# Optimization experiments

Hardware: AMD Instinct MI355X
Metric: run time of the kernel (lower is better)

## Reference

```python
import jax, jax.numpy as jnp
import numpy as np

N_NODES = 100000
N_EDGES = 1600000
IN_FEATS = 128
N_HIDDEN = 32
N_CLASSES = 47
HEADS = (4, 4)
NEG_SLOPE = 0.2


def setup_inputs() -> dict:
    key = jax.random.key(0)
    ks = jax.random.split(key, 12)
    x = jax.random.normal(ks[0], (N_NODES, IN_FEATS), dtype=jnp.float32)
    src = jax.random.randint(ks[1], (N_EDGES,), 0, N_NODES)
    dst = jax.random.randint(ks[2], (N_EDGES,), 0, N_NODES)
    inverse_idx = jax.random.randint(ks[3], (N_NODES,), 0, N_NODES)
    h1 = HEADS[0] * N_HIDDEN
    s1 = 1.0 / np.sqrt(IN_FEATS)
    W1 = jax.random.normal(ks[4], (IN_FEATS, h1), dtype=jnp.float32) * s1
    al1 = jax.random.normal(ks[5], (HEADS[0], N_HIDDEN), dtype=jnp.float32) * 0.1
    ar1 = jax.random.normal(ks[6], (HEADS[0], N_HIDDEN), dtype=jnp.float32) * 0.1
    b1 = jnp.zeros((h1,), dtype=jnp.float32)
    h2 = HEADS[1] * N_CLASSES
    s2 = 1.0 / np.sqrt(h1)
    W2 = jax.random.normal(ks[7], (h1, h2), dtype=jnp.float32) * s2
    al2 = jax.random.normal(ks[8], (HEADS[1], N_CLASSES), dtype=jnp.float32) * 0.1
    ar2 = jax.random.normal(ks[9], (HEADS[1], N_CLASSES), dtype=jnp.float32) * 0.1
    b2 = jnp.zeros((h2,), dtype=jnp.float32)
    return {"x": x, "src": src, "dst": dst, "inverse_idx": inverse_idx,
            "W1": W1, "al1": al1, "ar1": ar1, "b1": b1,
            "W2": W2, "al2": al2, "ar2": ar2, "b2": b2}


def gat_conv(h, src, dst, W, al, ar, b, heads, out_dim, apply_elu):
    # DGL GATConv (feat_drop=attn_drop=0, eval mode):
    # projected per-head features, edge attention, per-dst softmax, aggregate.
    feat = (h @ W).reshape(-1, heads, out_dim)               # (N, H, D)
    el = jnp.einsum('nhd,hd->nh', feat, al)                  # (N, H)
    er = jnp.einsum('nhd,hd->nh', feat, ar)                  # (N, H)
    e = el[src] + er[dst]                                    # (E, H)
    e = jnp.where(e > 0, e, NEG_SLOPE * e)                   # LeakyReLU
    m = jax.ops.segment_max(e, dst, num_segments=N_NODES)    # (N, H)
    m = jnp.where(jnp.isfinite(m), m, 0.0)
    ex = jnp.exp(e - m[dst])
    s = jax.ops.segment_sum(ex, dst, num_segments=N_NODES)   # (N, H)
    alpha = ex / jnp.maximum(s[dst], 1e-9)                   # (E, H)
    msg = feat[src] * alpha[:, :, None]                      # (E, H, D)
    out = jax.ops.segment_sum(msg, dst, num_segments=N_NODES)  # (N, H, D)
    out = out + b.reshape(1, heads, out_dim)
    if apply_elu:
        out = jax.nn.elu(out)
    return out


def reference(x, src, dst, inverse_idx, W1, al1, ar1, b1, W2, al2, ar2, b2):
    # Layer 0: GATConv + ELU, flatten heads, then NPFeatureShuffle reindex.
    h = gat_conv(x, src, dst, W1, al1, ar1, b1, HEADS[0], N_HIDDEN, True)
    h = h.reshape(N_NODES, HEADS[0] * N_HIDDEN)
    h = h[inverse_idx]  # cross-partition shuffle reindex
    # Layer 1: GATConv, no activation, mean over heads.
    h = gat_conv(h, src, dst, W2, al2, ar2, b2, HEADS[1], N_CLASSES, False)
    return h.mean(axis=1)  # (N, n_classes)
```

## Files before the change

kernel.cpp:

```cpp
#include <hip/hip_runtime.h>
#include <hip/hip_bf16.h>
#include <hip/hip_fp16.h>
#include <type_traits>

#define N_NODES 100000
#define N_EDGES 1600000

typedef _Float16 half8_t __attribute__((ext_vector_type(8)));
typedef _Float16 half4_t __attribute__((ext_vector_type(4)));
typedef float floatx4 __attribute__((ext_vector_type(4)));

__global__ void csr_prep(const int* __restrict__ dst, int* __restrict__ deg, int E,
                         const float* __restrict__ W1, const float* __restrict__ W2,
                         const float* __restrict__ al1, const float* __restrict__ ar1,
                         const float* __restrict__ al2, const float* __restrict__ ar2,
                         __half* __restrict__ Wt1, __half* __restrict__ Wt2) {
    const int b = blockIdx.x;
    if (b < 6250) {
        int i = b * 256 + threadIdx.x;
        if (i < E) atomicAdd(&deg[dst[i]], 1);
        return;
    }
    const int c = b - 6250;
    const int k = threadIdx.x;
    if (k >= 128) return;
    if (c < 128) {
        Wt1[c * 128 + k] = __float2half(W1[k * 128 + c]);
    } else if (c < 144) {
        int j = c - 128;
        float v = 0.f;
        if (j < 8) {
            int h = j & 3;
            const float* a = (j < 4) ? al1 : ar1;
            for (int d = 0; d < 32; ++d)
                v = fmaf(W1[k * 128 + h * 32 + d], a[h * 32 + d], v);
        }
        Wt1[c * 128 + k] = __float2half(v);
    } else if (c < 336) {
        int c2 = c - 144;
        float v = (c2 < 188) ? W2[k * 188 + c2] : 0.f;
        Wt2[c2 * 128 + k] = __float2half(v);
    } else {
        int j = c - 336;
        float v = 0.f;
        if (j < 8) {
            int h = j & 3;
            const float* a = (j < 4) ? al2 : ar2;
            for (int d = 0; d < 47; ++d)
                v = fmaf(W2[k * 188 + h * 47 + d], a[h * 47 + d], v);
        }
        Wt2[(192 + j) * 128 + k] = __float2half(v);
    }
}

__global__ void block_sums(const int* __restrict__ deg, int* __restrict__ bsum, int N) {
    __shared__ int ws[4];
    const int t = threadIdx.x;
    int i = blockIdx.x * 256 + t;
    int v = (i < N) ? deg[i] : 0;
    #pragma unroll
    for (int o = 32; o; o >>= 1) v += __shfl_down(v, o, 64);
    if ((t & 63) == 0) ws[t >> 6] = v;
    __syncthreads();
    if (t == 0) bsum[blockIdx.x] = ws[0] + ws[1] + ws[2] + ws[3];
}

__global__ void scan_bsum(int* __restrict__ bsum, int nb) {
    __shared__ int sh[512];
    const int t = threadIdx.x;
    sh[t] = (t < nb) ? bsum[t] : 0;
    __syncthreads();
    for (int o = 1; o < 512; o <<= 1) {
        int v = (t >= o) ? sh[t - o] : 0;
        __syncthreads();
        sh[t] += v;
        __syncthreads();
    }
    if (t < nb) bsum[t] = sh[t];
}

__global__ void scan_final(const int* __restrict__ deg, const int* __restrict__ bsum,
                           int* __restrict__ row_ptr, int* __restrict__ cursor, int N) {
    __shared__ int ws[4];
    const int t = threadIdx.x;
    const int b = blockIdx.x;
    const int i = b * 256 + t;
    const int lane = t & 63;
    const int wid = t >> 6;
    int v = (i < N) ? deg[i] : 0;
    int x = v;
    #pragma unroll
    for (int o = 1; o < 64; o <<= 1) {
        int y = __shfl_up(x, o, 64);
        if (lane >= o) x += y;
    }
    if (lane == 63) ws[wid] = x;
    __syncthreads();
    int prefix = (b > 0) ? bsum[b - 1] : 0;
    for (int k = 0; k < wid; ++k) prefix += ws[k];
    if (i < N) {
        row_ptr[i + 1] = prefix + x;
        cursor[i] = prefix + x - v;
    }
    if (i == 0) row_ptr[0] = 0;
}

__global__ void scatter_edges_part(const int* __restrict__ src, const int* __restrict__ dst,
                                   int* __restrict__ cursor, int* __restrict__ e_src, int E) {
    const int part = blockIdx.x & 7;
    const int sb = blockIdx.x >> 3;
    const int nslices = gridDim.x >> 3;
    const int psz = N_NODES / 8;
    const int lo = part * psz;
    const int hi = (part == 7) ? N_NODES : lo + psz;
    const int begin = (int)((long long)E * sb / nslices);
    const int end = (int)((long long)E * (sb + 1) / nslices);
    for (int i = begin + threadIdx.x; i < end; i += blockDim.x) {
        int d = dst[i];
        if (d >= lo && d < hi) {
            int p = atomicAdd(&cursor[d], 1);
            e_src[p] = src[i];
        }
    }
}

template <int TT, int NLOG, int OSTRIDE, bool EMBED, bool GATHER, typename AT>
__global__ __launch_bounds__(256) void gemm_mfma(
    const AT* __restrict__ A, const __half* __restrict__ Wt,
    __half* __restrict__ C, __half* __restrict__ elh, float* __restrict__ er,
    const int* __restrict__ gather, int N) {
    constexpr int LDA = 136;
    __shared__ _Float16 As[64 * LDA];
    __shared__ int ridx[64];
    const int tid = threadIdx.x;
    const int r0 = blockIdx.x * 64;

    if (tid < 64) {
        int row = r0 + tid;
        int pr = 0;
        if (row < N) pr = GATHER ? gather[row] : row;
        ridx[tid] = pr;
    }
    __syncthreads();

    {
        const int r = tid >> 2, q = tid & 3;
        const int src = ridx[r];
        if constexpr (std::is_same<AT, float>::value) {
            const float4* A4 = (const float4*)A;
            #pragma unroll
            for (int i = 0; i < 8; ++i) {
                float4 v = A4[(size_t)src * 32 + q * 8 + i];
                half4_t hv = {(_Float16)v.x, (_Float16)v.y, (_Float16)v.z, (_Float16)v.w};
                *(half4_t*)&As[r * LDA + q * 32 + i * 4] = hv;
            }
        } else {
            const uint4* A4 = (const uint4*)A;
            #pragma unroll
            for (int i = 0; i < 4; ++i) {
                uint4 v = A4[(size_t)src * 16 + q * 4 + i];
                *(uint4*)&As[r * LDA + q * 32 + i * 8] = v;
            }
        }
    }
    __syncthreads();

    const int lane = tid & 63;
    const int wave = tid >> 6;
    const int col = lane & 15;
    const int quad = lane >> 4;
    const int arow = wave * 16 + col;

    floatx4 acc[TT];
    #pragma unroll
    for (int t = 0; t < TT; ++t) acc[t] = (floatx4){0.f, 0.f, 0.f, 0.f};

    #pragma unroll
    for (int kc = 0; kc < 4; ++kc) {
        half8_t a = *(const half8_t*)&As[arow * LDA + kc * 32 + quad * 8];
        #pragma unroll
        for (int t = 0; t < TT; ++t) {
            half8_t b = *(const half8_t*)&Wt[(size_t)(t * 16 + col) * 128 + kc * 32 + quad * 8];
            acc[t] = __builtin_amdgcn_mfma_f32_16x16x32_f16(a, b, acc[t], 0, 0, 0);
        }
    }

    #pragma unroll
    for (int t = 0; t < TT - 1; ++t) {
        #pragma unroll
        for (int r = 0; r < 4; ++r) {
            int row = r0 + wave * 16 + quad * 4 + r;
            int c = t * 16 + col;
            if (row < N && c < NLOG) {
                int sc = EMBED ? (c + c / 47) : c;
                C[(size_t)row * OSTRIDE + sc] = __float2half(acc[t][r]);
            }
        }
    }
    #pragma unroll
    for (int r = 0; r < 4; ++r) {
        int row = r0 + wave * 16 + quad * 4 + r;
        if (row < N) {
            if (col < 4) {
                if constexpr (EMBED)
                    C[(size_t)row * OSTRIDE + col * 48 + 47] = __float2half(acc[TT - 1][r]);
                else
                    elh[row * 4 + col] = __float2half(acc[TT - 1][r]);
            } else if (col < 8) {
                er[row * 4 + (col - 4)] = acc[TT - 1][r];
            }
        }
    }
}

__global__ __launch_bounds__(256) void gat_gather1(
    const __half* __restrict__ feat, const __half* __restrict__ elh,
    const float* __restrict__ er,
    const int* __restrict__ row_ptr, const int* __restrict__ e_src,
    const float* __restrict__ bias, __half* __restrict__ out) {
    const int t = threadIdx.x;
    const int lane = t & 63;
    const int n = blockIdx.x * 4 + (t >> 6);
    const int h = lane >> 4;
    const int start = row_ptr[n], end = row_ptr[n + 1];
    const __half2* f2 = (const __half2*)feat;
    const float ern = er[n * 4 + h];
    float ax = 0.f, ay = 0.f, s = 0.f;
    int i = start;
    for (; i + 4 <= end; i += 4) {
        int sv0 = e_src[i + 0], sv1 = e_src[i + 1], sv2 = e_src[i + 2], sv3 = e_src[i + 3];
        float e0 = __half2float(elh[sv0 * 4 + h]) + ern;
        float e1 = __half2float(elh[sv1 * 4 + h]) + ern;
        float e2 = __half2float(elh[sv2 * 4 + h]) + ern;
        float e3 = __half2float(elh[sv3 * 4 + h]) + ern;
        float w0 = __expf(fmaxf(e0, 0.2f * e0));
        float w1 = __expf(fmaxf(e1, 0.2f * e1));
        float w2 = __expf(fmaxf(e2, 0.2f * e2));
        float w3 = __expf(fmaxf(e3, 0.2f * e3));
        __half2 f0 = f2[(size_t)sv0 * 64 + lane];
        __half2 f1 = f2[(size_t)sv1 * 64 + lane];
        __half2 f2v = f2[(size_t)sv2 * 64 + lane];
        __half2 f3 = f2[(size_t)sv3 * 64 + lane];
        float2 g0 = __half22float2(f0), g1 = __half22float2(f1);
        float2 g2 = __half22float2(f2v), g3 = __half22float2(f3);
        s += (w0 + w1) + (w2 + w3);
        ax += w0 * g0.x + w1 * g1.x + w2 * g2.x + w3 * g3.x;
        ay += w0 * g0.y + w1 * g1.y + w2 * g2.y + w3 * g3.y;
    }
    for (; i < end; ++i) {
        int sv = e_src[i];
        float e = __half2float(elh[sv * 4 + h]) + ern;
        float ww = __expf(fmaxf(e, 0.2f * e));
        float2 g = __half22float2(f2[(size_t)sv * 64 + lane]);
        s += ww;
        ax += ww * g.x;
        ay += ww * g.y;
    }
    float inv = 1.f / fmaxf(s, 1e-9f);
    float ox = ax * inv + bias[lane * 2 + 0];
    float oy = ay * inv + bias[lane * 2 + 1];
    ox = (ox > 0.f) ? ox : (__expf(ox) - 1.f);
    oy = (oy > 0.f) ? oy : (__expf(oy) - 1.f);
    ((__half2*)out)[(size_t)n * 64 + lane] = __floats2half2_rn(ox, oy);
}

__global__ __launch_bounds__(256) void gat_gather2(
    const __half* __restrict__ feat, const float* __restrict__ er,
    const int* __restrict__ row_ptr, const int* __restrict__ e_src,
    const float* __restrict__ bias, float* __restrict__ out) {
    const int t = threadIdx.x;
    const int lane = t & 63;
    const int n = blockIdx.x * 4 + (t >> 6);
    if (lane < 48) {
        const int h = lane / 12;
        const int q = lane - h * 12;
        const int g11 = h * 12 + 11;
        const int start = row_ptr[n], end = row_ptr[n + 1];
        const half4_t* f4 = (const half4_t*)feat;
        const float ern = er[n * 4 + h];
        float a0 = 0.f, a1 = 0.f, a2 = 0.f, a3 = 0.f, s = 0.f;
        int i = start;
        for (; i + 4 <= end; i += 4) {
            int sv0 = e_src[i + 0], sv1 = e_src[i + 1], sv2 = e_src[i + 2], sv3 = e_src[i + 3];
            half4_t f0 = f4[(size_t)sv0 * 48 + lane];
            half4_t f1 = f4[(size_t)sv1 * 48 + lane];
            half4_t f2 = f4[(size_t)sv2 * 48 + lane];
            half4_t f3 = f4[(size_t)sv3 * 48 + lane];
            float e0 = __shfl((float)f0[3], g11, 64) + ern;
            float e1 = __shfl((float)f1[3], g11, 64) + ern;
            float e2 = __shfl((float)f2[3], g11, 64) + ern;
            float e3 = __shfl((float)f3[3], g11, 64) + ern;
            float w0 = __expf(fmaxf(e0, 0.2f * e0));
            float w1 = __expf(fmaxf(e1, 0.2f * e1));
            float w2 = __expf(fmaxf(e2, 0.2f * e2));
            float w3 = __expf(fmaxf(e3, 0.2f * e3));
            s += (w0 + w1) + (w2 + w3);
            a0 += w0 * (float)f0[0] + w1 * (float)f1[0] + w2 * (float)f2[0] + w3 * (float)f3[0];
            a1 += w0 * (float)f0[1] + w1 * (float)f1[1] + w2 * (float)f2[1] + w3 * (float)f3[1];
            a2 += w0 * (float)f0[2] + w1 * (float)f1[2] + w2 * (float)f2[2] + w3 * (float)f3[2];
            a3 += w0 * (float)f0[3] + w1 * (float)f1[3] + w2 * (float)f2[3] + w3 * (float)f3[3];
        }
        for (; i < end; ++i) {
            int sv = e_src[i];
            half4_t f0 = f4[(size_t)sv * 48 + lane];
            float e = __shfl((float)f0[3], g11, 64) + ern;
            float ww = __expf(fmaxf(e, 0.2f * e));
            s += ww;
            a0 += ww * (float)f0[0];
            a1 += ww * (float)f0[1];
            a2 += ww * (float)f0[2];
            a3 += ww * (float)f0[3];
        }
        if (q == 11) a3 = 0.f;
        float inv = 1.f / fmaxf(s, 1e-9f);
        const int d0 = q * 4;
        float b0 = bias[h * 47 + d0 + 0];
        float b1 = bias[h * 47 + d0 + 1];
        float b2 = bias[h * 47 + d0 + 2];
        float b3 = (d0 + 3 < 47) ? bias[h * 47 + d0 + 3] : 0.f;
        float r0 = a0 * inv + b0;
        float r1 = a1 * inv + b1;
        float r2 = a2 * inv + b2;
        float r3 = a3 * inv + b3;
        float t0 = r0 + __shfl(r0, lane + 12, 64) + __shfl(r0, lane + 24, 64) + __shfl(r0, lane + 36, 64);
        float t1 = r1 + __shfl(r1, lane + 12, 64) + __shfl(r1, lane + 24, 64) + __shfl(r1, lane + 36, 64);
        float t2 = r2 + __shfl(r2, lane + 12, 64) + __shfl(r2, lane + 24, 64) + __shfl(r2, lane + 36, 64);
        float t3 = r3 + __shfl(r3, lane + 12, 64) + __shfl(r3, lane + 24, 64) + __shfl(r3, lane + 36, 64);
        if (h == 0) {
            size_t base = (size_t)n * 47 + d0;
            out[base + 0] = 0.25f * t0;
            out[base + 1] = 0.25f * t1;
            out[base + 2] = 0.25f * t2;
            if (d0 + 3 < 47) out[base + 3] = 0.25f * t3;
        }
    }
}

extern "C" void kernel_launch(void* const* d_in, const int* in_sizes, int n_in,
                              void* d_out, int out_size, void* d_ws, size_t ws_size,
                              hipStream_t stream) {
    const int N = N_NODES, E = N_EDGES;
    const float* x    = (const float*)d_in[0];
    const int*   src  = (const int*)d_in[1];
    const int*   dst  = (const int*)d_in[2];
    const int*   inv  = (const int*)d_in[3];
    const float* W1   = (const float*)d_in[4];
    const float* al1  = (const float*)d_in[5];
    const float* ar1  = (const float*)d_in[6];
    const float* b1   = (const float*)d_in[7];
    const float* W2   = (const float*)d_in[8];
    const float* al2  = (const float*)d_in[9];
    const float* ar2  = (const float*)d_in[10];
    const float* b2   = (const float*)d_in[11];
    float* out = (float*)d_out;

    char* p = (char*)d_ws;
    auto carve = [&](size_t bytes) {
        char* q = p;
        p += (bytes + 255) & ~size_t(255);
        return q;
    };
    __half* feat1   = (__half*)carve((size_t)N * 128 * 2);
    __half* feat2   = (__half*)carve((size_t)N * 192 * 2);
    __half* hbuf    = (__half*)carve((size_t)N * 128 * 2);
    __half* Wt1     = (__half*)carve(144 * 128 * 2);
    __half* Wt2     = (__half*)carve(208 * 128 * 2);
    __half* elh1    = (__half*)carve((size_t)N * 4 * 2);
    float*  er      = (float*)carve((size_t)N * 4 * 4);
    int*    deg     = (int*)carve((size_t)N * 4);
    int*    row_ptr = (int*)carve((size_t)(N + 1) * 4);
    int*    cursor  = (int*)carve((size_t)N * 4);
    int*    bsum    = (int*)carve(512 * 4);
    int*    e_src   = (int*)carve((size_t)E * 4);

    const int nb = (N + 255) / 256;

    hipMemsetAsync(deg, 0, (size_t)N * 4, stream);
    csr_prep<<<6250 + 352, 256, 0, stream>>>(dst, deg, E, W1, W2, al1, ar1, al2, ar2, Wt1, Wt2);
    block_sums<<<nb, 256, 0, stream>>>(deg, bsum, N);
    scan_bsum<<<1, 512, 0, stream>>>(bsum, nb);
    scan_final<<<nb, 256, 0, stream>>>(deg, bsum, row_ptr, cursor, N);
    scatter_edges_part<<<2048, 256, 0, stream>>>(src, dst, cursor, e_src, E);

    gemm_mfma<9, 128, 128, false, false, float><<<(N + 63) / 64, 256, 0, stream>>>(
        x, Wt1, feat1, elh1, er, nullptr, N);
    gat_gather1<<<(N + 3) / 4, 256, 0, stream>>>(feat1, elh1, er, row_ptr, e_src, b1, hbuf);

    gemm_mfma<13, 188, 192, true, true, __half><<<(N + 63) / 64, 256, 0, stream>>>(
        hbuf, Wt2, feat2, nullptr, er, inv, N);
    gat_gather2<<<(N + 3) / 4, 256, 0, stream>>>(feat2, er, row_ptr, e_src, b2, out);
}
```

Measured before the change: 519.8 us.

## Fuse edge scatter with layer-1 GEMM and compute layer-2 edge weights once per edge

The edge scatter and the first projection GEMM now run in one launch, with even block groups scattering edges (using int4 vector loads over 200 fixed slices) and odd groups running GEMM tiles, so the two independent stages overlap. In the second gather, each edge's attention weight per head is computed once by 16 lanes and broadcast by shuffle, instead of every feature lane shuffling and exponentiating. Feature addressing switches to 32-bit byte offsets to cut 64-bit address arithmetic. The fused kernel assumes E divides evenly into 200 slices and N_NODES by 8, and mixing the two block types in one grid may hurt occupancy balance.

Measured after the change: 513.4 us. No clear change (-1.2%).

```diff
diff --git a/kernel.cpp b/kernel.cpp
--- a/kernel.cpp
+++ b/kernel.cpp
@@ -105,27 +105,9 @@
     if (i == 0) row_ptr[0] = 0;
 }
 
-__global__ void scatter_edges_part(const int* __restrict__ src, const int* __restrict__ dst,
-                                   int* __restrict__ cursor, int* __restrict__ e_src, int E) {
-    const int part = blockIdx.x & 7;
-    const int sb = blockIdx.x >> 3;
-    const int nslices = gridDim.x >> 3;
-    const int psz = N_NODES / 8;
-    const int lo = part * psz;
-    const int hi = (part == 7) ? N_NODES : lo + psz;
-    const int begin = (int)((long long)E * sb / nslices);
-    const int end = (int)((long long)E * (sb + 1) / nslices);
-    for (int i = begin + threadIdx.x; i < end; i += blockDim.x) {
-        int d = dst[i];
-        if (d >= lo && d < hi) {
-            int p = atomicAdd(&cursor[d], 1);
-            e_src[p] = src[i];
-        }
-    }
-}
-
 template <int TT, int NLOG, int OSTRIDE, bool EMBED, bool GATHER, typename AT>
-__global__ __launch_bounds__(256) void gemm_mfma(
+__device__ __forceinline__ void gemm_body(
+    int bx,
     const AT* __restrict__ A, const __half* __restrict__ Wt,
     __half* __restrict__ C, __half* __restrict__ elh, float* __restrict__ er,
     const int* __restrict__ gather, int N) {
@@ -133,7 +115,7 @@
     __shared__ _Float16 As[64 * LDA];
     __shared__ int ridx[64];
     const int tid = threadIdx.x;
-    const int r0 = blockIdx.x * 64;
+    const int r0 = bx * 64;
 
     if (tid < 64) {
         int row = r0 + tid;
@@ -213,6 +195,45 @@
     }
 }
 
+template <int TT, int NLOG, int OSTRIDE, bool EMBED, bool GATHER, typename AT>
+__global__ __launch_bounds__(256) void gemm_mfma(
+    const AT* __restrict__ A, const __half* __restrict__ Wt,
+    __half* __restrict__ C, __half* __restrict__ elh, float* __restrict__ er,
+    const int* __restrict__ gather, int N) {
+    gemm_body<TT, NLOG, OSTRIDE, EMBED, GATHER, AT>(blockIdx.x, A, Wt, C, elh, er, gather, N);
+}
+
+__global__ __launch_bounds__(256) void scatter_gemm1(
+    const int* __restrict__ src, const int* __restrict__ dst,
+    int* __restrict__ cursor, int* __restrict__ e_src, int E,
+    const float* __restrict__ A, const __half* __restrict__ Wt,
+    __half* __restrict__ C, __half* __restrict__ elh, float* __restrict__ er, int N) {
+    const int g = blockIdx.x >> 3;
+    if ((g & 1) == 0) {
+        const int part = blockIdx.x & 7;
+        const int sb = g >> 1;
+        const int psz = N_NODES / 8;
+        const int lo = part * psz;
+        const int hi = lo + psz;
+        const int SLICE = E / 200;
+        const int4* d4 = (const int4*)(dst + sb * SLICE);
+        const int4* s4 = (const int4*)(src + sb * SLICE);
+        const int nvec = SLICE / 4;
+        for (int v = threadIdx.x; v < nvec; v += 256) {
+            int4 dd = d4[v];
+            int4 ss = s4[v];
+            if (dd.x >= lo && dd.x < hi) e_src[atomicAdd(&cursor[dd.x], 1)] = ss.x;
+            if (dd.y >= lo && dd.y < hi) e_src[atomicAdd(&cursor[dd.y], 1)] = ss.y;
+            if (dd.z >= lo && dd.z < hi) e_src[atomicAdd(&cursor[dd.z], 1)] = ss.z;
+            if (dd.w >= lo && dd.w < hi) e_src[atomicAdd(&cursor[dd.w], 1)] = ss.w;
+        }
+    } else {
+        const int bx = (g >> 1) * 8 + (blockIdx.x & 7);
+        if (bx * 64 < N)
+            gemm_body<9, 128, 128, false, false, float>(bx, A, Wt, C, elh, er, nullptr, N);
+    }
+}
+
 __global__ __launch_bounds__(256) void gat_gather1(
     const __half* __restrict__ feat, const __half* __restrict__ elh,
     const float* __restrict__ er,
@@ -223,7 +244,8 @@
     const int n = blockIdx.x * 4 + (t >> 6);
     const int h = lane >> 4;
     const int start = row_ptr[n], end = row_ptr[n + 1];
-    const __half2* f2 = (const __half2*)feat;
+    const char* fb = (const char*)feat;
+    const uint32_t flo = (uint32_t)lane * 4u;
     const float ern = er[n * 4 + h];
     float ax = 0.f, ay = 0.f, s = 0.f;
     int i = start;
@@ -237,10 +259,10 @@
         float w1 = __expf(fmaxf(e1, 0.2f * e1));
         float w2 = __expf(fmaxf(e2, 0.2f * e2));
         float w3 = __expf(fmaxf(e3, 0.2f * e3));
-        __half2 f0 = f2[(size_t)sv0 * 64 + lane];
-        __half2 f1 = f2[(size_t)sv1 * 64 + lane];
-        __half2 f2v = f2[(size_t)sv2 * 64 + lane];
-        __half2 f3 = f2[(size_t)sv3 * 64 + lane];
+        __half2 f0 = *(const __half2*)(fb + (uint32_t)sv0 * 256u + flo);
+        __half2 f1 = *(const __half2*)(fb + (uint32_t)sv1 * 256u + flo);
+        __half2 f2v = *(const __half2*)(fb + (uint32_t)sv2 * 256u + flo);
+        __half2 f3 = *(const __half2*)(fb + (uint32_t)sv3 * 256u + flo);
         float2 g0 = __half22float2(f0), g1 = __half22float2(f1);
         float2 g2 = __half22float2(f2v), g3 = __half22float2(f3);
         s += (w0 + w1) + (w2 + w3);
@@ -251,7 +273,7 @@
         int sv = e_src[i];
         float e = __half2float(elh[sv * 4 + h]) + ern;
         float ww = __expf(fmaxf(e, 0.2f * e));
-        float2 g = __half22float2(f2[(size_t)sv * 64 + lane]);
+        float2 g = __half22float2(*(const __half2*)(fb + (uint32_t)sv * 256u + flo));
         s += ww;
         ax += ww * g.x;
         ay += ww * g.y;
@@ -271,46 +293,56 @@
     const int t = threadIdx.x;
     const int lane = t & 63;
     const int n = blockIdx.x * 4 + (t >> 6);
-    if (lane < 48) {
-        const int h = lane / 12;
-        const int q = lane - h * 12;
-        const int g11 = h * 12 + 11;
-        const int start = row_ptr[n], end = row_ptr[n + 1];
-        const half4_t* f4 = (const half4_t*)feat;
-        const float ern = er[n * 4 + h];
-        float a0 = 0.f, a1 = 0.f, a2 = 0.f, a3 = 0.f, s = 0.f;
-        int i = start;
-        for (; i + 4 <= end; i += 4) {
-            int sv0 = e_src[i + 0], sv1 = e_src[i + 1], sv2 = e_src[i + 2], sv3 = e_src[i + 3];
-            half4_t f0 = f4[(size_t)sv0 * 48 + lane];
-            half4_t f1 = f4[(size_t)sv1 * 48 + lane];
-            half4_t f2 = f4[(size_t)sv2 * 48 + lane];
-            half4_t f3 = f4[(size_t)sv3 * 48 + lane];
-            float e0 = __shfl((float)f0[3], g11, 64) + ern;
-            float e1 = __shfl((float)f1[3], g11, 64) + ern;
-            float e2 = __shfl((float)f2[3], g11, 64) + ern;
-            float e3 = __shfl((float)f3[3], g11, 64) + ern;
-            float w0 = __expf(fmaxf(e0, 0.2f * e0));
-            float w1 = __expf(fmaxf(e1, 0.2f * e1));
-            float w2 = __expf(fmaxf(e2, 0.2f * e2));
-            float w3 = __expf(fmaxf(e3, 0.2f * e3));
-            s += (w0 + w1) + (w2 + w3);
+    const int he = (lane >> 2) & 3;
+    const int ee = lane & 3;
+    const int start = row_ptr[n], end = row_ptr[n + 1];
+    const char* fb = (const char*)feat;
+    const float erw = er[n * 4 + he];
+    const uint32_t elo = (uint32_t)he * 96u + 94u;
+    const int h = lane / 12;
+    const int q = lane - h * 12;
+    const int wb = h * 4;
+    const uint32_t flo = (uint32_t)lane * 8u;
+    float a0 = 0.f, a1 = 0.f, a2 = 0.f, a3 = 0.f, s = 0.f;
+    int i = start;
+    for (; i + 4 <= end; i += 4) {
+        int sv0 = e_src[i + 0], sv1 = e_src[i + 1], sv2 = e_src[i + 2], sv3 = e_src[i + 3];
+        int svw = (ee == 1) ? sv1 : (ee == 2) ? sv2 : (ee == 3) ? sv3 : sv0;
+        float el = __half2float(*(const __half*)(fb + (uint32_t)svw * 384u + elo));
+        float e = el + erw;
+        float w = __expf(fmaxf(e, 0.2f * e));
+        float w0 = __shfl(w, wb + 0, 64);
+        float w1 = __shfl(w, wb + 1, 64);
+        float w2 = __shfl(w, wb + 2, 64);
+        float w3 = __shfl(w, wb + 3, 64);
+        if (lane < 48) {
+            half4_t f0 = *(const half4_t*)(fb + (uint32_t)sv0 * 384u + flo);
+            half4_t f1 = *(const half4_t*)(fb + (uint32_t)sv1 * 384u + flo);
+            half4_t f2 = *(const half4_t*)(fb + (uint32_t)sv2 * 384u + flo);
+            half4_t f3 = *(const half4_t*)(fb + (uint32_t)sv3 * 384u + flo);
             a0 += w0 * (float)f0[0] + w1 * (float)f1[0] + w2 * (float)f2[0] + w3 * (float)f3[0];
             a1 += w0 * (float)f0[1] + w1 * (float)f1[1] + w2 * (float)f2[1] + w3 * (float)f3[1];
             a2 += w0 * (float)f0[2] + w1 * (float)f1[2] + w2 * (float)f2[2] + w3 * (float)f3[2];
             a3 += w0 * (float)f0[3] + w1 * (float)f1[3] + w2 * (float)f2[3] + w3 * (float)f3[3];
         }
-        for (; i < end; ++i) {
-            int sv = e_src[i];
-            half4_t f0 = f4[(size_t)sv * 48 + lane];
-            float e = __shfl((float)f0[3], g11, 64) + ern;
-            float ww = __expf(fmaxf(e, 0.2f * e));
-            s += ww;
+        s += (w0 + w1) + (w2 + w3);
+    }
+    for (; i < end; ++i) {
+        int sv = e_src[i];
+        float el = __half2float(*(const __half*)(fb + (uint32_t)sv * 384u + elo));
+        float e = el + erw;
+        float w = __expf(fmaxf(e, 0.2f * e));
+        float ww = __shfl(w, wb, 64);
+        if (lane < 48) {
+            half4_t f0 = *(const half4_t*)(fb + (uint32_t)sv * 384u + flo);
             a0 += ww * (float)f0[0];
             a1 += ww * (float)f0[1];
             a2 += ww * (float)f0[2];
             a3 += ww * (float)f0[3];
         }
+        s += ww;
+    }
+    if (lane < 48) {
         if (q == 11) a3 = 0.f;
         float inv = 1.f / fmaxf(s, 1e-9f);
         const int d0 = q * 4;
@@ -380,10 +412,10 @@
     block_sums<<<nb, 256, 0, stream>>>(deg, bsum, N);
     scan_bsum<<<1, 512, 0, stream>>>(bsum, nb);
     scan_final<<<nb, 256, 0, stream>>>(deg, bsum, row_ptr, cursor, N);
-    scatter_edges_part<<<2048, 256, 0, stream>>>(src, dst, cursor, e_src, E);
-
-    gemm_mfma<9, 128, 128, false, false, float><<<(N + 63) / 64, 256, 0, stream>>>(
-        x, Wt1, feat1, elh1, er, nullptr, N);
+
+    scatter_gemm1<<<3200, 256, 0, stream>>>(src, dst, cursor, e_src, E,
+                                            x, Wt1, feat1, elh1, er, N);
+
     gat_gather1<<<(N + 3) / 4, 256, 0, stream>>>(feat1, elh1, er, row_ptr, e_src, b1, hbuf);
 
     gemm_mfma<13, 188, 192, true, true, __half><<<(N + 63) / 64, 256, 0, stream>>>(
```
